# Optimization experiments

Measured on AMD Instinct MI355X. Metric: run time of the kernel, lower is better.

Reference implementation:

```python
import jax, jax.numpy as jnp
import numpy as np

Nknn = 10
Np = 20
N = 524288
DOWN, LEFT, RIGHT, UP, WIDTH = -5.0, -5.0, 5.0, 5.0, 1.0


def setup_inputs() -> dict:
    key = jax.random.key(0)
    ks = jax.random.split(key, 20)
    def p(k, shape, fan_in):
        return jax.random.normal(k, shape, jnp.float32) / jnp.sqrt(jnp.float32(fan_in))
    inp = {
        "t": jax.random.uniform(ks[0], (1,), jnp.float32),
        "y": jax.random.normal(ks[1], (N, 4 + 2 * Np), jnp.float32),
        # net1: Linear(4,8) -> ReLU -> Linear(8,2)
        "w1a": p(ks[2], (4, 8), 4),   "b1a": p(ks[3], (8,), 4),
        "w1b": p(ks[4], (8, 2), 8),   "b1b": p(ks[5], (2,), 8),
        # net2: Linear(1,16) -> ReLU -> Linear(16,8) -> ReLU -> Linear(8,1)
        "w2a": p(ks[6], (1, 16), 1),  "b2a": p(ks[7], (16,), 1),
        "w2b": p(ks[8], (16, 8), 16), "b2b": p(ks[9], (8,), 16),
        "w2c": p(ks[10], (8, 1), 8),  "b2c": p(ks[11], (1,), 8),
        # net3: same architecture as net2
        "w3a": p(ks[12], (1, 16), 1), "b3a": p(ks[13], (16,), 1),
        "w3b": p(ks[14], (16, 8), 16),"b3b": p(ks[15], (8,), 16),
        "w3c": p(ks[16], (8, 1), 8),  "b3c": p(ks[17], (1,), 8),
    }
    return inp


def _mlp3(x, wa, ba, wb, bb, wc, bc):
    # Linear -> ReLU -> Linear -> ReLU -> Linear, applied on last axis
    h = jax.nn.relu(x @ wa + ba)
    h = jax.nn.relu(h @ wb + bb)
    return h @ wc + bc


def reference(t, y, w1a, b1a, w1b, b1b, w2a, b2a, w2b, b2b, w2c, b2c,
              w3a, b3a, w3b, b3b, w3c, b3c):
    y = y.astype(jnp.float32)
    theX = y[:, 0:2]            # positions [N,2]
    theV = y[:, 2:4]            # velocities [N,2]
    ux = y[:, 4:4 + 2 * Nknn].reshape(-1, Nknn, 2)  # neighbor offsets [N,Nknn,2]

    dxdt = theV

    # goal-attraction term f1
    door = jnp.array([RIGHT + 0.6, 0.0], jnp.float32)
    diff = door - theX
    unit_e = diff / jnp.sqrt(jnp.sum(diff * diff, axis=1, keepdims=True))
    h = jax.nn.relu(jnp.concatenate([unit_e, theV], axis=1) @ w1a + b1a)
    f1 = h @ w1b + b1b          # [N,2]

    # wall-repulsion term f2; rows inside the door gap get rightdist=100
    x0 = theX[:, 0:1]
    x1 = theX[:, 1:2]
    rightdist = jnp.where((x1 < WIDTH) & (x1 > -WIDTH), 100.0, RIGHT - x0)
    wall_in = jnp.stack([x0 - LEFT, x1 - DOWN, UP - x1, rightdist], axis=1)  # [N,4,1]
    o = _mlp3(wall_in, w2a, b2a, w2b, bb=b2b, wc=w2c, bc=b2c) if False else _mlp3(wall_in, w2a, b2a, w2b, b2b, w2c, b2c)  # [N,4,1]
    # directions: [1,0], [0,1], [0,-1], [-1,0]
    f2 = jnp.concatenate([o[:, 0] - o[:, 3], o[:, 1] - o[:, 2]], axis=1)  # [N,2]

    # neighbor-repulsion term f3 (vectorized over Nknn)
    d = jnp.sqrt(jnp.sum(ux * ux, axis=2, keepdims=True))  # [N,Nknn,1]
    f3 = -jnp.sum(_mlp3(d, w3a, b3a, w3b, b3b, w3c, b3c) * ux / d, axis=1)  # [N,2]

    dvdt = (f1 + f2 + f3) / 80.0
    dudt = jnp.zeros((y.shape[0], 2 * Nknn), y.dtype)
    result = jnp.concatenate([dxdt, dvdt, dudt], axis=1)  # [N, 4 + 2*Nknn]

    # zero out agents that have exited (x > RIGHT)
    result = jnp.where((theX[:, 0] > RIGHT)[:, None], 0.0, result)
    return result
```

## Files before the change

kernel.cpp:

```cpp
#include <hip/hip_runtime.h>

#define NROW  524288
#define BLK   256
#define NKNN  10
#define YCOLS 44
#define OCOLS 24

#define TBL    256
#define T2_LO  (-2.0f)
#define T3_LO  (0.0f)
#define T_H    (1.0f / 16.0f)
#define T_INVH 16.0f

__device__ __forceinline__ float mlp_scalar_g(float s,
    const float* __restrict__ wa, const float* __restrict__ ba,
    const float* __restrict__ wb, const float* __restrict__ bb,
    const float* __restrict__ wc, const float* __restrict__ bc) {
    float h[16];
#pragma unroll
    for (int j = 0; j < 16; ++j)
        h[j] = fmaxf(fmaf(s, wa[j], ba[j]), 0.0f);
    float g[8];
#pragma unroll
    for (int k = 0; k < 8; ++k) g[k] = bb[k];
#pragma unroll
    for (int j = 0; j < 16; ++j) {
        float hj = h[j];
#pragma unroll
        for (int k = 0; k < 8; ++k)
            g[k] = fmaf(hj, wb[j * 8 + k], g[k]);
    }
    float o = bc[0];
#pragma unroll
    for (int k = 0; k < 8; ++k)
        o = fmaf(fmaxf(g[k], 0.0f), wc[k], o);
    return o;
}

__device__ __forceinline__ float tbl_eval(const float* __restrict__ T, float s, float lo) {
    float u = (s - lo) * T_INVH;
    u = fminf(fmaxf(u, 0.0f), (float)TBL - 1.001f);
    int i = (int)u;
    float f = u - (float)i;
    float va = T[i];
    float vb = T[i + 1];
    return fmaf(f, vb - va, va);
}

__global__ __launch_bounds__(BLK) void odefunc_kernel(
    const float* __restrict__ y,
    const float* __restrict__ w1a, const float* __restrict__ b1a,
    const float* __restrict__ w1b, const float* __restrict__ b1b,
    const float* __restrict__ w2a, const float* __restrict__ b2a,
    const float* __restrict__ w2b, const float* __restrict__ b2b,
    const float* __restrict__ w2c, const float* __restrict__ b2c,
    const float* __restrict__ w3a, const float* __restrict__ b3a,
    const float* __restrict__ w3b, const float* __restrict__ b3b,
    const float* __restrict__ w3c, const float* __restrict__ b3c,
    float* __restrict__ out)
{
    __shared__ float4 S[BLK * 6];
    __shared__ float  T2v[TBL];
    __shared__ float  T3v[TBL];
    __shared__ float  o100s;

    const int t = threadIdx.x;

    const float4* yb = reinterpret_cast<const float4*>(y) + (size_t)blockIdx.x * BLK * (YCOLS / 4);
    float4 ld[6];
#pragma unroll
    for (int i = 0; i < 6; ++i) {
        int j  = t + i * BLK;
        int rr = j / 6;
        int cc = j - rr * 6;
        ld[i] = yb[rr * 11 + cc];
    }

    {
        float s2 = T2_LO + (float)t * T_H;
        T2v[t] = mlp_scalar_g(s2, w2a, b2a, w2b, b2b, w2c, b2c);
        float s3 = T3_LO + (float)t * T_H;
        T3v[t] = mlp_scalar_g(s3, w3a, b3a, w3b, b3b, w3c, b3c);
        if (t == 0)
            o100s = mlp_scalar_g(100.0f, w2a, b2a, w2b, b2b, w2c, b2c);
    }

#pragma unroll
    for (int i = 0; i < 6; ++i)
        S[t + i * BLK] = ld[i];
    __syncthreads();

    float4 a  = S[t * 6 + 0];
    float4 u0 = S[t * 6 + 1];
    float4 u1 = S[t * 6 + 2];
    float4 u2 = S[t * 6 + 3];
    float4 u3 = S[t * 6 + 4];
    float4 u4 = S[t * 6 + 5];
    const float o100 = o100s;

    float dx = 5.6f - a.x;
    float dy = 0.0f - a.y;
    float inv = rsqrtf(fmaf(dx, dx, dy * dy));
    float in1[4] = { dx * inv, dy * inv, a.z, a.w };
    float h1[8];
#pragma unroll
    for (int j = 0; j < 8; ++j) {
        float s = b1a[j];
#pragma unroll
        for (int k = 0; k < 4; ++k)
            s = fmaf(in1[k], w1a[k * 8 + j], s);
        h1[j] = fmaxf(s, 0.0f);
    }
    float f1x = b1b[0];
    float f1y = b1b[1];
#pragma unroll
    for (int j = 0; j < 8; ++j) {
        f1x = fmaf(h1[j], w1b[j * 2 + 0], f1x);
        f1y = fmaf(h1[j], w1b[j * 2 + 1], f1y);
    }

    bool corridor = (a.y < 1.0f) && (a.y > -1.0f);
    float o0 = tbl_eval(T2v, a.x + 5.0f, T2_LO);
    float o1 = tbl_eval(T2v, a.y + 5.0f, T2_LO);
    float o2 = tbl_eval(T2v, 5.0f - a.y, T2_LO);
    float o3 = corridor ? o100 : tbl_eval(T2v, 5.0f - a.x, T2_LO);
    float f2x = o0 - o3;
    float f2y = o1 - o2;

    float us[2 * NKNN] = { u0.x, u0.y, u0.z, u0.w,
                           u1.x, u1.y, u1.z, u1.w,
                           u2.x, u2.y, u2.z, u2.w,
                           u3.x, u3.y, u3.z, u3.w,
                           u4.x, u4.y, u4.z, u4.w };
    float f3x = 0.0f, f3y = 0.0f;
#pragma unroll
    for (int n = 0; n < NKNN; ++n) {
        float uxn = us[2 * n + 0];
        float uyn = us[2 * n + 1];
        float s2  = fmaf(uxn, uxn, uyn * uyn);
        float idn = rsqrtf(s2);
        float d   = s2 * idn;
        float m   = tbl_eval(T3v, d, T3_LO);
        float c   = m * idn;
        f3x = fmaf(-c, uxn, f3x);
        f3y = fmaf(-c, uyn, f3y);
    }

    bool dead = (a.x > 5.0f);
    const float k80 = 1.0f / 80.0f;
    float4 r;
    r.x = dead ? 0.0f : a.z;
    r.y = dead ? 0.0f : a.w;
    r.z = dead ? 0.0f : (f1x + f2x + f3x) * k80;
    r.w = dead ? 0.0f : (f1y + f2y + f3y) * k80;

    const float4 z = make_float4(0.0f, 0.0f, 0.0f, 0.0f);
    S[t * 6 + 0] = r;
    S[t * 6 + 1] = z;
    S[t * 6 + 2] = z;
    S[t * 6 + 3] = z;
    S[t * 6 + 4] = z;
    S[t * 6 + 5] = z;
    __syncthreads();

    float4* o4 = reinterpret_cast<float4*>(out) + (size_t)blockIdx.x * BLK * (OCOLS / 4);
#pragma unroll
    for (int i = 0; i < 6; ++i)
        o4[t + i * BLK] = S[t + i * BLK];
}

extern "C" void kernel_launch(void* const* d_in, const int* in_sizes, int n_in,
                              void* d_out, int out_size, void* d_ws, size_t ws_size,
                              hipStream_t stream) {
    int iy = 1;
    for (int i = 0; i < n_in; ++i) {
        if (in_sizes[i] == NROW * YCOLS) { iy = i; break; }
    }
    const float* y   = (const float*)d_in[iy];
    const float* w1a = (const float*)d_in[iy + 1];
    const float* b1a = (const float*)d_in[iy + 2];
    const float* w1b = (const float*)d_in[iy + 3];
    const float* b1b = (const float*)d_in[iy + 4];
    const float* w2a = (const float*)d_in[iy + 5];
    const float* b2a = (const float*)d_in[iy + 6];
    const float* w2b = (const float*)d_in[iy + 7];
    const float* b2b = (const float*)d_in[iy + 8];
    const float* w2c = (const float*)d_in[iy + 9];
    const float* b2c = (const float*)d_in[iy + 10];
    const float* w3a = (const float*)d_in[iy + 11];
    const float* b3a = (const float*)d_in[iy + 12];
    const float* w3b = (const float*)d_in[iy + 13];
    const float* b3b = (const float*)d_in[iy + 14];
    const float* w3c = (const float*)d_in[iy + 15];
    const float* b3c = (const float*)d_in[iy + 16];
    float* out = (float*)d_out;

    hipLaunchKernelGGL(odefunc_kernel, dim3(NROW / BLK), dim3(BLK), 0, stream,
                       y, w1a, b1a, w1b, b1b,
                       w2a, b2a, w2b, b2b, w2c, b2c,
                       w3a, b3a, w3b, b3b, w3c, b3c, out);
}
```

Before: 31.45 us.

## Make LDS row transpose wave-local and use nontemporal output stores

Each wave now loads and transposes only its own 64 rows through shared memory. This replaces the two block-wide barriers around the staging with wave barriers, leaving one block barrier for the lookup tables. Output stores use nontemporal hints so the write-only result does not pollute the cache. The risk is that LDS hazards are only ordered within the wave, which depends on the wave barrier semantics being sufficient.

```diff
diff --git a/kernel.cpp b/kernel.cpp
--- a/kernel.cpp
+++ b/kernel.cpp
@@ -11,6 +11,8 @@
 #define T3_LO  (0.0f)
 #define T_H    (1.0f / 16.0f)
 #define T_INVH 16.0f
+
+typedef float f32x4 __attribute__((ext_vector_type(4)));
 
 __device__ __forceinline__ float mlp_scalar_g(float s,
     const float* __restrict__ wa, const float* __restrict__ ba,
@@ -59,43 +61,45 @@
     const float* __restrict__ w3c, const float* __restrict__ b3c,
     float* __restrict__ out)
 {
-    __shared__ float4 S[BLK * 6];
-    __shared__ float  T2v[TBL];
-    __shared__ float  T3v[TBL];
-    __shared__ float  o100s;
-
-    const int t = threadIdx.x;
-
-    const float4* yb = reinterpret_cast<const float4*>(y) + (size_t)blockIdx.x * BLK * (YCOLS / 4);
-    float4 ld[6];
+    __shared__ f32x4 S[BLK * 6];
+    __shared__ float T2v[TBL];
+    __shared__ float T3v[TBL];
+    __shared__ float o100s;
+
+    const int t    = threadIdx.x;
+    const int w    = t >> 6;
+    const int lane = t & 63;
+
+    const f32x4* yb = reinterpret_cast<const f32x4*>(y) + (size_t)blockIdx.x * BLK * (YCOLS / 4);
+    f32x4 ld[6];
+    int jj[6];
 #pragma unroll
     for (int i = 0; i < 6; ++i) {
-        int j  = t + i * BLK;
+        int j  = lane + i * 64;
         int rr = j / 6;
         int cc = j - rr * 6;
-        ld[i] = yb[rr * 11 + cc];
-    }
-
-    {
-        float s2 = T2_LO + (float)t * T_H;
-        T2v[t] = mlp_scalar_g(s2, w2a, b2a, w2b, b2b, w2c, b2c);
-        float s3 = T3_LO + (float)t * T_H;
-        T3v[t] = mlp_scalar_g(s3, w3a, b3a, w3b, b3b, w3c, b3c);
-        if (t == 0)
-            o100s = mlp_scalar_g(100.0f, w2a, b2a, w2b, b2b, w2c, b2c);
-    }
+        jj[i]  = j;
+        ld[i]  = yb[(64 * w + rr) * 11 + cc];
+    }
+
+    T2v[t] = mlp_scalar_g(T2_LO + (float)t * T_H, w2a, b2a, w2b, b2b, w2c, b2c);
+    T3v[t] = mlp_scalar_g(T3_LO + (float)t * T_H, w3a, b3a, w3b, b3b, w3c, b3c);
+    if (t == 0)
+        o100s = mlp_scalar_g(100.0f, w2a, b2a, w2b, b2b, w2c, b2c);
+
+    __syncthreads();
 
 #pragma unroll
     for (int i = 0; i < 6; ++i)
-        S[t + i * BLK] = ld[i];
-    __syncthreads();
-
-    float4 a  = S[t * 6 + 0];
-    float4 u0 = S[t * 6 + 1];
-    float4 u1 = S[t * 6 + 2];
-    float4 u2 = S[t * 6 + 3];
-    float4 u3 = S[t * 6 + 4];
-    float4 u4 = S[t * 6 + 5];
+        S[384 * w + jj[i]] = ld[i];
+    __builtin_amdgcn_wave_barrier();
+
+    f32x4 a  = S[t * 6 + 0];
+    f32x4 u0 = S[t * 6 + 1];
+    f32x4 u1 = S[t * 6 + 2];
+    f32x4 u2 = S[t * 6 + 3];
+    f32x4 u3 = S[t * 6 + 4];
+    f32x4 u4 = S[t * 6 + 5];
     const float o100 = o100s;
 
     float dx = 5.6f - a.x;
@@ -148,25 +152,28 @@
 
     bool dead = (a.x > 5.0f);
     const float k80 = 1.0f / 80.0f;
-    float4 r;
+    f32x4 r;
     r.x = dead ? 0.0f : a.z;
     r.y = dead ? 0.0f : a.w;
     r.z = dead ? 0.0f : (f1x + f2x + f3x) * k80;
     r.w = dead ? 0.0f : (f1y + f2y + f3y) * k80;
 
-    const float4 z = make_float4(0.0f, 0.0f, 0.0f, 0.0f);
+    const f32x4 z = (f32x4)(0.0f);
     S[t * 6 + 0] = r;
     S[t * 6 + 1] = z;
     S[t * 6 + 2] = z;
     S[t * 6 + 3] = z;
     S[t * 6 + 4] = z;
     S[t * 6 + 5] = z;
-    __syncthreads();
-
-    float4* o4 = reinterpret_cast<float4*>(out) + (size_t)blockIdx.x * BLK * (OCOLS / 4);
-#pragma unroll
-    for (int i = 0; i < 6; ++i)
-        o4[t + i * BLK] = S[t + i * BLK];
+    __builtin_amdgcn_wave_barrier();
+
+    f32x4* o4 = reinterpret_cast<f32x4*>(out) + (size_t)blockIdx.x * BLK * (OCOLS / 4);
+#pragma unroll
+    for (int i = 0; i < 6; ++i) {
+        int j = 384 * w + lane + i * 64;
+        f32x4 v = S[j];
+        __builtin_nontemporal_store(v, &o4[j]);
+    }
 }
 
 extern "C" void kernel_launch(void* const* d_in, const int* in_sizes, int n_in,
```

After: 30.48 us. -3.1%, faster.
